# Kernel tuning notes

Hardware: AMD Instinct MI355X
Metric: run time of the kernel (lower is better)

The kernel has to match this reference:

```python
import jax, jax.numpy as jnp
import numpy as np

NUM_QUERIES = 256  # num_queries init arg
D = 256            # decoder_dim


def fps(xyz, n):
    """Furthest point sampling, matching the CUDA furthest_point_sample kernel:
    start at index 0, keep running min squared distance, pick argmax each step.
    xyz: [B, N, 3] -> indices [B, n] int32."""
    B, N, _ = xyz.shape

    def step(carry, _):
        dist, far = carry
        centroid = jnp.take_along_axis(xyz, far[:, None, None], axis=1)  # [B,1,3]
        d = jnp.sum((xyz - centroid) ** 2, axis=-1)                      # [B,N]
        dist = jnp.minimum(dist, d)
        return (dist, jnp.argmax(dist, axis=-1).astype(jnp.int32)), far

    init = (jnp.full((B, N), 1e10, xyz.dtype), jnp.zeros((B,), jnp.int32))
    _, inds = jax.lax.scan(step, init, None, length=n)
    return jnp.transpose(inds)  # [B, n]


def setup_inputs() -> dict:
    key = jax.random.key(0)
    ks = jax.random.split(key, 6)
    B, N = 64, 32768
    # scene coords in roughly [-3, 3]^3 meters
    encoder_xyz = jax.random.uniform(ks[0], (B, N, 3), jnp.float32) * 6.0 - 3.0
    pc_min = jnp.min(encoder_xyz, axis=1)  # [B,3]
    pc_max = jnp.max(encoder_xyz, axis=1)  # [B,3]
    gauss_B = jax.random.normal(ks[1], (3, D // 2), jnp.float32)  # fourier freqs
    W1 = jax.random.normal(ks[2], (D, D), jnp.float32) / np.sqrt(D)
    b1 = jnp.zeros((D,), jnp.float32)
    W2 = jax.random.normal(ks[3], (D, D), jnp.float32) / np.sqrt(D)
    b2 = jnp.zeros((D,), jnp.float32)
    return dict(encoder_xyz=encoder_xyz, pc_min=pc_min, pc_max=pc_max,
                gauss_B=gauss_B, W1=W1, b1=b1, W2=W2, b2=b2)


def reference(encoder_xyz, pc_min, pc_max, gauss_B, W1, b1, W2, b2):
    # --- query selection: FPS + gather (indices are non-differentiable) ---
    inds = fps(jax.lax.stop_gradient(encoder_xyz), NUM_QUERIES)          # [B,nq]
    query_xyz = jnp.take_along_axis(encoder_xyz, inds[..., None], axis=1)  # [B,nq,3]
    # --- PositionEmbeddingCoordsSine (fourier, normalize=True) ---
    norm = (query_xyz - pc_min[:, None, :]) / (pc_max - pc_min)[:, None, :]
    proj = (2.0 * jnp.pi) * jnp.einsum('bnd,df->bnf', norm, gauss_B)     # [B,nq,D/2]
    pos = jnp.concatenate([jnp.sin(proj), jnp.cos(proj)], axis=-1)       # [B,nq,D]
    pos = jnp.transpose(pos, (0, 2, 1))                                   # [B,D,nq]
    # --- query_projection GenericMLP: conv1x1 + ReLU, conv1x1 + output ReLU ---
    h = jax.nn.relu(jnp.einsum('bcn,dc->bdn', pos, W1) + b1[:, None])
    query_embed = jax.nn.relu(jnp.einsum('bcn,dc->bdn', h, W2) + b2[:, None])
    return query_xyz, query_embed
```

## Files before the change

### kernel.cpp

```cpp
#include <hip/hip_runtime.h>

#define FPS_N 32768
#define FPS_T 256
#define NBLK 8
#define PPB (FPS_N / NBLK)
#define PPT (PPB / FPS_T)
#define NCH (PPT / 4)
#define NQ 256
#define DD 256
#define B_BATCH 64
#define FPS_BLOCKS (B_BATCH * NBLK)
#define EMB_BLOCKS (B_BATCH * 4)
#define CHQ 16
#define PLP 20

#define WS_CLEAR_BYTES (B_BATCH * NQ * NBLK * 8)

__global__ __attribute__((amdgpu_flat_work_group_size(FPS_T, FPS_T),
                          amdgpu_waves_per_eu(2, 2)))
void fps_embed_kernel(const float* __restrict__ xyz,
                      const float* __restrict__ pcmin,
                      const float* __restrict__ pcmax,
                      const float* __restrict__ G,
                      const float* __restrict__ W1, const float* __restrict__ b1,
                      const float* __restrict__ W2, const float* __restrict__ b2,
                      float* __restrict__ qout, float* __restrict__ eout,
                      unsigned long long* __restrict__ gslot) {
  const int gid = blockIdx.x;
  const int t = threadIdx.x;

  __shared__ unsigned long long sred[FPS_T / 64];
  __shared__ float4 bc;
  __shared__ __align__(16) float Pl[DD][PLP];
  __shared__ __align__(16) float Hl[DD][PLP];
  __shared__ int swidx[CHQ];
  __shared__ float snrm[CHQ][3];

  if (gid < FPS_BLOCKS) {
    const int xcd = gid & 7;
    const int s = gid >> 3;
    const int b = xcd + 8 * (s >> 3);
    const int q = s & 7;

    const float* __restrict__ base = xyz + (size_t)b * (FPS_N * 3);
    const float4* __restrict__ base4 =
        (const float4*)(base + (size_t)q * PPB * 3) + (size_t)t * (PPT * 3 / 4);
    float* qb = qout + (size_t)b * (NQ * 3);
    unsigned long long* bslot = gslot + (size_t)b * (NQ * NBLK);

    float4 C[PPT * 3 / 4];
#pragma unroll
    for (int i = 0; i < PPT * 3 / 4; ++i) C[i] = base4[i];
#pragma unroll
    for (int i = 0; i < PPT * 3 / 4; ++i) {
      asm volatile("" : "+v"(C[i].x), "+v"(C[i].y), "+v"(C[i].z), "+v"(C[i].w));
    }
    float4 Dst[NCH];
#pragma unroll
    for (int c = 0; c < NCH; ++c) Dst[c] = make_float4(1e10f, 1e10f, 1e10f, 1e10f);

    if (q == 0 && t == 0) { qb[0] = base[0]; qb[1] = base[1]; qb[2] = base[2]; }
    float cx = base[0], cy = base[1], cz = base[2];

#pragma unroll 1
    for (int j = 1; j < NQ; ++j) {
      float best = -1.0f;
      int bik = 0;

#pragma unroll
      for (int c = 0; c < NCH; ++c) {
        const float4 a4 = C[3 * c + 0];
        const float4 b4 = C[3 * c + 1];
        const float4 c4 = C[3 * c + 2];
        const float px[4] = {a4.x, a4.w, b4.z, c4.y};
        const float py[4] = {a4.y, b4.x, b4.w, c4.z};
        const float pz[4] = {a4.z, b4.y, c4.x, c4.w};
        const float dold[4] = {Dst[c].x, Dst[c].y, Dst[c].z, Dst[c].w};
        float dnew[4];
#pragma unroll
        for (int i = 0; i < 4; ++i) {
          const float dx = __fsub_rn(px[i], cx);
          const float dy = __fsub_rn(py[i], cy);
          const float dz = __fsub_rn(pz[i], cz);
          const float d = __fadd_rn(__fadd_rn(__fmul_rn(dx, dx), __fmul_rn(dy, dy)),
                                    __fmul_rn(dz, dz));
          const float nd = fminf(dold[i], d);
          dnew[i] = nd;
          if (nd > best) { best = nd; bik = c * 4 + i; }
        }
        Dst[c] = make_float4(dnew[0], dnew[1], dnew[2], dnew[3]);
      }
      int bi = q * PPB + t * PPT + bik;

#pragma unroll
      for (int off = 32; off; off >>= 1) {
        const float ov = __shfl_xor(best, off);
        const int oi = __shfl_xor(bi, off);
        if (ov > best || (ov == best && oi < bi)) { best = ov; bi = oi; }
      }
      if ((t & 63) == 0) {
        sred[t >> 6] = ((unsigned long long)(unsigned int)__float_as_int(best) << 32) |
                       (unsigned int)~(unsigned int)bi;
      }
      __syncthreads();

      if (t < 64) {
        unsigned long long p = sred[t & 3];
#pragma unroll
        for (int off = 1; off < 4; off <<= 1) {
          const unsigned long long o = __shfl_xor(p, off);
          if (o > p) p = o;
        }
        if (t == 0) {
          __hip_atomic_store(&bslot[j * NBLK + q], p, __ATOMIC_RELAXED,
                             __HIP_MEMORY_SCOPE_AGENT);
        }
        unsigned long long rp = 0;
        if (t < NBLK) {
          const unsigned long long* sl = &bslot[j * NBLK + t];
          do {
            rp = __hip_atomic_load(sl, __ATOMIC_RELAXED, __HIP_MEMORY_SCOPE_AGENT);
          } while (rp == 0ull);
        }
#pragma unroll
        for (int off = 1; off < NBLK; off <<= 1) {
          const unsigned long long o = __shfl_xor(rp, off);
          if (o > rp) rp = o;
        }
        if (t == 0) {
          const int gi = (int)~(unsigned int)(rp & 0xffffffffull);
          const float* cp = base + 3 * (size_t)gi;
          const float ncx = cp[0], ncy = cp[1], ncz = cp[2];
          bc = make_float4(ncx, ncy, ncz, 0.f);
          if (q == 0) { qb[3 * j + 0] = ncx; qb[3 * j + 1] = ncy; qb[3 * j + 2] = ncz; }
        }
      }
      __syncthreads();
      cx = bc.x; cy = bc.y; cz = bc.z;
    }
  } else {
    const int eid = gid - FPS_BLOCKS;
    const int b = eid >> 2;
    const int n0 = (eid & 3) * 64;
    const float* __restrict__ base = xyz + (size_t)b * (FPS_N * 3);
    unsigned long long* bslot = gslot + (size_t)b * (NQ * NBLK);
    float* ob = eout + (size_t)b * (DD * NQ);

    const float mn0 = pcmin[3 * b + 0], mn1 = pcmin[3 * b + 1], mn2 = pcmin[3 * b + 2];
    const float mx0 = pcmax[3 * b + 0], mx1 = pcmax[3 * b + 1], mx2 = pcmax[3 * b + 2];
    const int ty = t >> 2, tx = t & 3;

#pragma unroll 1
    for (int ch = 0; ch < 64 / CHQ; ++ch) {
      const int j0 = n0 + ch * CHQ;
      if (t < NBLK) {
        const unsigned long long* sl = &bslot[(size_t)(j0 + CHQ - 1) * NBLK + t];
        while (__hip_atomic_load(sl, __ATOMIC_RELAXED,
                                 __HIP_MEMORY_SCOPE_AGENT) == 0ull) {
          __builtin_amdgcn_s_sleep(2);
        }
      }
      __syncthreads();
      unsigned long long p = 0xffffffffull;
      if (t < 128) {
        const int line = j0 + (t >> 3);
        if (line > 0) {
          p = __hip_atomic_load(&bslot[(size_t)line * NBLK + (t & 7)],
                                __ATOMIC_RELAXED, __HIP_MEMORY_SCOPE_AGENT);
        }
      }
#pragma unroll
      for (int off = 1; off < 8; off <<= 1) {
        const unsigned long long o = __shfl_xor(p, off);
        if (o > p) p = o;
      }
      if (t < 128 && (t & 7) == 0) {
        swidx[t >> 3] = (int)~(unsigned int)(p & 0xffffffffull);
      }
      __syncthreads();
      if (t < CHQ) {
        const int gi = swidx[t];
        snrm[t][0] = (base[3 * gi + 0] - mn0) / (mx0 - mn0);
        snrm[t][1] = (base[3 * gi + 1] - mn1) / (mx1 - mn1);
        snrm[t][2] = (base[3 * gi + 2] - mn2) / (mx2 - mn2);
      }
      __syncthreads();
      {
        const int qi = t & 15;
        const int fb = t >> 4;
        const float nx = snrm[qi][0], ny = snrm[qi][1], nz = snrm[qi][2];
#pragma unroll
        for (int it = 0; it < 8; ++it) {
          const int f = fb + it * 16;
          const float sfv = nx * G[f] + ny * G[128 + f] + nz * G[256 + f];
          const float pr = 6.28318530717958647692f * sfv;
          Pl[f][qi] = sinf(pr);
          Pl[f + 128][qi] = cosf(pr);
        }
      }
      __syncthreads();
      {
        float acc[4][4] = {};
        const float* wr0 = W1 + (size_t)(ty * 4 + 0) * DD;
        const float* wr1 = wr0 + DD;
        const float* wr2 = wr1 + DD;
        const float* wr3 = wr2 + DD;
#pragma unroll 2
        for (int c = 0; c < DD; c += 4) {
          const float4 a0 = *(const float4*)(wr0 + c);
          const float4 a1 = *(const float4*)(wr1 + c);
          const float4 a2 = *(const float4*)(wr2 + c);
          const float4 a3 = *(const float4*)(wr3 + c);
          const float4 p0 = *(const float4*)&Pl[c + 0][tx * 4];
          const float4 p1 = *(const float4*)&Pl[c + 1][tx * 4];
          const float4 p2 = *(const float4*)&Pl[c + 2][tx * 4];
          const float4 p3 = *(const float4*)&Pl[c + 3][tx * 4];
          const float av[4][4] = {{a0.x, a0.y, a0.z, a0.w},
                                  {a1.x, a1.y, a1.z, a1.w},
                                  {a2.x, a2.y, a2.z, a2.w},
                                  {a3.x, a3.y, a3.z, a3.w}};
          const float pv[4][4] = {{p0.x, p0.y, p0.z, p0.w},
                                  {p1.x, p1.y, p1.z, p1.w},
                                  {p2.x, p2.y, p2.z, p2.w},
                                  {p3.x, p3.y, p3.z, p3.w}};
#pragma unroll
          for (int cj = 0; cj < 4; ++cj)
#pragma unroll
            for (int i = 0; i < 4; ++i)
#pragma unroll
              for (int k = 0; k < 4; ++k)
                acc[i][k] = fmaf(av[i][cj], pv[cj][k], acc[i][k]);
        }
#pragma unroll
        for (int i = 0; i < 4; ++i) {
          const float bv = b1[ty * 4 + i];
          float4 h;
          h.x = fmaxf(acc[i][0] + bv, 0.f);
          h.y = fmaxf(acc[i][1] + bv, 0.f);
          h.z = fmaxf(acc[i][2] + bv, 0.f);
          h.w = fmaxf(acc[i][3] + bv, 0.f);
          *(float4*)&Hl[ty * 4 + i][tx * 4] = h;
        }
      }
      __syncthreads();
      {
        float acc[4][4] = {};
        const float* wr0 = W2 + (size_t)(ty * 4 + 0) * DD;
        const float* wr1 = wr0 + DD;
        const float* wr2 = wr1 + DD;
        const float* wr3 = wr2 + DD;
#pragma unroll 2
        for (int c = 0; c < DD; c += 4) {
          const float4 a0 = *(const float4*)(wr0 + c);
          const float4 a1 = *(const float4*)(wr1 + c);
          const float4 a2 = *(const float4*)(wr2 + c);
          const float4 a3 = *(const float4*)(wr3 + c);
          const float4 p0 = *(const float4*)&Hl[c + 0][tx * 4];
          const float4 p1 = *(const float4*)&Hl[c + 1][tx * 4];
          const float4 p2 = *(const float4*)&Hl[c + 2][tx * 4];
          const float4 p3 = *(const float4*)&Hl[c + 3][tx * 4];
          const float av[4][4] = {{a0.x, a0.y, a0.z, a0.w},
                                  {a1.x, a1.y, a1.z, a1.w},
                                  {a2.x, a2.y, a2.z, a2.w},
                                  {a3.x, a3.y, a3.z, a3.w}};
          const float pv[4][4] = {{p0.x, p0.y, p0.z, p0.w},
                                  {p1.x, p1.y, p1.z, p1.w},
                                  {p2.x, p2.y, p2.z, p2.w},
                                  {p3.x, p3.y, p3.z, p3.w}};
#pragma unroll
          for (int cj = 0; cj < 4; ++cj)
#pragma unroll
            for (int i = 0; i < 4; ++i)
#pragma unroll
              for (int k = 0; k < 4; ++k)
                acc[i][k] = fmaf(av[i][cj], pv[cj][k], acc[i][k]);
        }
#pragma unroll
        for (int i = 0; i < 4; ++i) {
          const float bv = b2[ty * 4 + i];
          float4 h;
          h.x = fmaxf(acc[i][0] + bv, 0.f);
          h.y = fmaxf(acc[i][1] + bv, 0.f);
          h.z = fmaxf(acc[i][2] + bv, 0.f);
          h.w = fmaxf(acc[i][3] + bv, 0.f);
          *(float4*)(ob + (size_t)(ty * 4 + i) * NQ + j0 + tx * 4) = h;
        }
      }
      __syncthreads();
    }
  }
}

extern "C" void kernel_launch(void* const* d_in, const int* in_sizes, int n_in,
                              void* d_out, int out_size, void* d_ws, size_t ws_size,
                              hipStream_t stream) {
  (void)in_sizes; (void)n_in; (void)ws_size; (void)out_size;
  const float* xyz   = (const float*)d_in[0];
  const float* pcmin = (const float*)d_in[1];
  const float* pcmax = (const float*)d_in[2];
  const float* G     = (const float*)d_in[3];
  const float* W1    = (const float*)d_in[4];
  const float* b1    = (const float*)d_in[5];
  const float* W2    = (const float*)d_in[6];
  const float* b2    = (const float*)d_in[7];

  float* qxyz  = (float*)d_out;
  float* embed = qxyz + (size_t)B_BATCH * NQ * 3;

  unsigned long long* gslot = (unsigned long long*)d_ws;

  hipMemsetAsync(d_ws, 0, WS_CLEAR_BYTES, stream);

  hipLaunchKernelGGL(fps_embed_kernel, dim3(FPS_BLOCKS + EMB_BLOCKS),
                     dim3(FPS_T), 0, stream, xyz, pcmin, pcmax, G,
                     W1, b1, W2, b2, qxyz, embed, gslot);
}
```

Baseline: 622.4 us.

## Split fused FPS+embedding kernel into separate FPS and MLP kernels

Replaces the single persistent kernel, where embedding blocks spin-waited on FPS progress slots to overlap the MLP with sampling, with two sequential launches. The FPS kernel now has only its own 512 blocks and no co-resident embedding blocks competing for CUs. The MLP kernel reads the query xyz from the output buffer and processes one 16-query chunk per block across 1024 blocks. This gives up the overlap of MLP work with FPS and adds a second launch, in exchange for removing the polling and contention from the FPS critical path.

```diff
diff --git a/kernel.cpp b/kernel.cpp
--- a/kernel.cpp
+++ b/kernel.cpp
@@ -9,8 +9,6 @@
 #define NQ 256
 #define DD 256
 #define B_BATCH 64
-#define FPS_BLOCKS (B_BATCH * NBLK)
-#define EMB_BLOCKS (B_BATCH * 4)
 #define CHQ 16
 #define PLP 20
 
@@ -18,275 +16,244 @@
 
 __global__ __attribute__((amdgpu_flat_work_group_size(FPS_T, FPS_T),
                           amdgpu_waves_per_eu(2, 2)))
-void fps_embed_kernel(const float* __restrict__ xyz,
-                      const float* __restrict__ pcmin,
-                      const float* __restrict__ pcmax,
-                      const float* __restrict__ G,
-                      const float* __restrict__ W1, const float* __restrict__ b1,
-                      const float* __restrict__ W2, const float* __restrict__ b2,
-                      float* __restrict__ qout, float* __restrict__ eout,
-                      unsigned long long* __restrict__ gslot) {
+void fps_kernel(const float* __restrict__ xyz, float* __restrict__ qout,
+                unsigned long long* __restrict__ gslot) {
   const int gid = blockIdx.x;
+  const int xcd = gid & 7;
+  const int s = gid >> 3;
+  const int b = xcd + 8 * (s >> 3);
+  const int q = s & 7;
   const int t = threadIdx.x;
+
+  const float* __restrict__ base = xyz + (size_t)b * (FPS_N * 3);
+  const float4* __restrict__ base4 =
+      (const float4*)(base + (size_t)q * PPB * 3) + (size_t)t * (PPT * 3 / 4);
+  float* qb = qout + (size_t)b * (NQ * 3);
+  unsigned long long* bslot = gslot + (size_t)b * (NQ * NBLK);
 
   __shared__ unsigned long long sred[FPS_T / 64];
   __shared__ float4 bc;
+
+  float4 C[PPT * 3 / 4];
+#pragma unroll
+  for (int i = 0; i < PPT * 3 / 4; ++i) C[i] = base4[i];
+#pragma unroll
+  for (int i = 0; i < PPT * 3 / 4; ++i) {
+    asm volatile("" : "+v"(C[i].x), "+v"(C[i].y), "+v"(C[i].z), "+v"(C[i].w));
+  }
+  float4 Dst[NCH];
+#pragma unroll
+  for (int c = 0; c < NCH; ++c) Dst[c] = make_float4(1e10f, 1e10f, 1e10f, 1e10f);
+
+  if (q == 0 && t == 0) { qb[0] = base[0]; qb[1] = base[1]; qb[2] = base[2]; }
+  float cx = base[0], cy = base[1], cz = base[2];
+
+#pragma unroll 1
+  for (int j = 1; j < NQ; ++j) {
+    float best = -1.0f;
+    int bik = 0;
+
+#pragma unroll
+    for (int c = 0; c < NCH; ++c) {
+      const float4 a4 = C[3 * c + 0];
+      const float4 b4 = C[3 * c + 1];
+      const float4 c4 = C[3 * c + 2];
+      const float px[4] = {a4.x, a4.w, b4.z, c4.y};
+      const float py[4] = {a4.y, b4.x, b4.w, c4.z};
+      const float pz[4] = {a4.z, b4.y, c4.x, c4.w};
+      const float dold[4] = {Dst[c].x, Dst[c].y, Dst[c].z, Dst[c].w};
+      float dnew[4];
+#pragma unroll
+      for (int i = 0; i < 4; ++i) {
+        const float dx = __fsub_rn(px[i], cx);
+        const float dy = __fsub_rn(py[i], cy);
+        const float dz = __fsub_rn(pz[i], cz);
+        const float d = __fadd_rn(__fadd_rn(__fmul_rn(dx, dx), __fmul_rn(dy, dy)),
+                                  __fmul_rn(dz, dz));
+        const float nd = fminf(dold[i], d);
+        dnew[i] = nd;
+        if (nd > best) { best = nd; bik = c * 4 + i; }
+      }
+      Dst[c] = make_float4(dnew[0], dnew[1], dnew[2], dnew[3]);
+    }
+    int bi = q * PPB + t * PPT + bik;
+
+#pragma unroll
+    for (int off = 32; off; off >>= 1) {
+      const float ov = __shfl_xor(best, off);
+      const int oi = __shfl_xor(bi, off);
+      if (ov > best || (ov == best && oi < bi)) { best = ov; bi = oi; }
+    }
+    if ((t & 63) == 0) {
+      sred[t >> 6] = ((unsigned long long)(unsigned int)__float_as_int(best) << 32) |
+                     (unsigned int)~(unsigned int)bi;
+    }
+    __syncthreads();
+
+    if (t < 64) {
+      unsigned long long p = sred[t & 3];
+#pragma unroll
+      for (int off = 1; off < 4; off <<= 1) {
+        const unsigned long long o = __shfl_xor(p, off);
+        if (o > p) p = o;
+      }
+      if (t == 0) {
+        __hip_atomic_store(&bslot[j * NBLK + q], p, __ATOMIC_RELAXED,
+                           __HIP_MEMORY_SCOPE_AGENT);
+      }
+      unsigned long long rp = 0;
+      if (t < NBLK) {
+        const unsigned long long* sl = &bslot[j * NBLK + t];
+        do {
+          rp = __hip_atomic_load(sl, __ATOMIC_RELAXED, __HIP_MEMORY_SCOPE_AGENT);
+        } while (rp == 0ull);
+      }
+#pragma unroll
+      for (int off = 1; off < NBLK; off <<= 1) {
+        const unsigned long long o = __shfl_xor(rp, off);
+        if (o > rp) rp = o;
+      }
+      if (t == 0) {
+        const int gi = (int)~(unsigned int)(rp & 0xffffffffull);
+        const float* cp = base + 3 * (size_t)gi;
+        const float ncx = cp[0], ncy = cp[1], ncz = cp[2];
+        bc = make_float4(ncx, ncy, ncz, 0.f);
+        if (q == 0) { qb[3 * j + 0] = ncx; qb[3 * j + 1] = ncy; qb[3 * j + 2] = ncz; }
+      }
+    }
+    __syncthreads();
+    cx = bc.x; cy = bc.y; cz = bc.z;
+  }
+}
+
+__global__ __launch_bounds__(256) void embed_mlp_kernel(
+    const float* __restrict__ qxyz, const float* __restrict__ pcmin,
+    const float* __restrict__ pcmax, const float* __restrict__ G,
+    const float* __restrict__ W1, const float* __restrict__ b1,
+    const float* __restrict__ W2, const float* __restrict__ b2,
+    float* __restrict__ out) {
+  const int eid = blockIdx.x;
+  const int b = eid >> 4;
+  const int j0 = (eid & 15) * CHQ;
+  const int t = threadIdx.x;
+  const int ty = t >> 2, tx = t & 3;
+
   __shared__ __align__(16) float Pl[DD][PLP];
   __shared__ __align__(16) float Hl[DD][PLP];
-  __shared__ int swidx[CHQ];
   __shared__ float snrm[CHQ][3];
 
-  if (gid < FPS_BLOCKS) {
-    const int xcd = gid & 7;
-    const int s = gid >> 3;
-    const int b = xcd + 8 * (s >> 3);
-    const int q = s & 7;
-
-    const float* __restrict__ base = xyz + (size_t)b * (FPS_N * 3);
-    const float4* __restrict__ base4 =
-        (const float4*)(base + (size_t)q * PPB * 3) + (size_t)t * (PPT * 3 / 4);
-    float* qb = qout + (size_t)b * (NQ * 3);
-    unsigned long long* bslot = gslot + (size_t)b * (NQ * NBLK);
-
-    float4 C[PPT * 3 / 4];
-#pragma unroll
-    for (int i = 0; i < PPT * 3 / 4; ++i) C[i] = base4[i];
-#pragma unroll
-    for (int i = 0; i < PPT * 3 / 4; ++i) {
-      asm volatile("" : "+v"(C[i].x), "+v"(C[i].y), "+v"(C[i].z), "+v"(C[i].w));
-    }
-    float4 Dst[NCH];
-#pragma unroll
-    for (int c = 0; c < NCH; ++c) Dst[c] = make_float4(1e10f, 1e10f, 1e10f, 1e10f);
-
-    if (q == 0 && t == 0) { qb[0] = base[0]; qb[1] = base[1]; qb[2] = base[2]; }
-    float cx = base[0], cy = base[1], cz = base[2];
-
-#pragma unroll 1
-    for (int j = 1; j < NQ; ++j) {
-      float best = -1.0f;
-      int bik = 0;
-
-#pragma unroll
-      for (int c = 0; c < NCH; ++c) {
-        const float4 a4 = C[3 * c + 0];
-        const float4 b4 = C[3 * c + 1];
-        const float4 c4 = C[3 * c + 2];
-        const float px[4] = {a4.x, a4.w, b4.z, c4.y};
-        const float py[4] = {a4.y, b4.x, b4.w, c4.z};
-        const float pz[4] = {a4.z, b4.y, c4.x, c4.w};
-        const float dold[4] = {Dst[c].x, Dst[c].y, Dst[c].z, Dst[c].w};
-        float dnew[4];
-#pragma unroll
-        for (int i = 0; i < 4; ++i) {
-          const float dx = __fsub_rn(px[i], cx);
-          const float dy = __fsub_rn(py[i], cy);
-          const float dz = __fsub_rn(pz[i], cz);
-          const float d = __fadd_rn(__fadd_rn(__fmul_rn(dx, dx), __fmul_rn(dy, dy)),
-                                    __fmul_rn(dz, dz));
-          const float nd = fminf(dold[i], d);
-          dnew[i] = nd;
-          if (nd > best) { best = nd; bik = c * 4 + i; }
-        }
-        Dst[c] = make_float4(dnew[0], dnew[1], dnew[2], dnew[3]);
-      }
-      int bi = q * PPB + t * PPT + bik;
-
-#pragma unroll
-      for (int off = 32; off; off >>= 1) {
-        const float ov = __shfl_xor(best, off);
-        const int oi = __shfl_xor(bi, off);
-        if (ov > best || (ov == best && oi < bi)) { best = ov; bi = oi; }
-      }
-      if ((t & 63) == 0) {
-        sred[t >> 6] = ((unsigned long long)(unsigned int)__float_as_int(best) << 32) |
-                       (unsigned int)~(unsigned int)bi;
-      }
-      __syncthreads();
-
-      if (t < 64) {
-        unsigned long long p = sred[t & 3];
-#pragma unroll
-        for (int off = 1; off < 4; off <<= 1) {
-          const unsigned long long o = __shfl_xor(p, off);
-          if (o > p) p = o;
-        }
-        if (t == 0) {
-          __hip_atomic_store(&bslot[j * NBLK + q], p, __ATOMIC_RELAXED,
-                             __HIP_MEMORY_SCOPE_AGENT);
-        }
-        unsigned long long rp = 0;
-        if (t < NBLK) {
-          const unsigned long long* sl = &bslot[j * NBLK + t];
-          do {
-            rp = __hip_atomic_load(sl, __ATOMIC_RELAXED, __HIP_MEMORY_SCOPE_AGENT);
-          } while (rp == 0ull);
-        }
-#pragma unroll
-        for (int off = 1; off < NBLK; off <<= 1) {
-          const unsigned long long o = __shfl_xor(rp, off);
-          if (o > rp) rp = o;
-        }
-        if (t == 0) {
-          const int gi = (int)~(unsigned int)(rp & 0xffffffffull);
-          const float* cp = base + 3 * (size_t)gi;
-          const float ncx = cp[0], ncy = cp[1], ncz = cp[2];
-          bc = make_float4(ncx, ncy, ncz, 0.f);
-          if (q == 0) { qb[3 * j + 0] = ncx; qb[3 * j + 1] = ncy; qb[3 * j + 2] = ncz; }
-        }
-      }
-      __syncthreads();
-      cx = bc.x; cy = bc.y; cz = bc.z;
-    }
-  } else {
-    const int eid = gid - FPS_BLOCKS;
-    const int b = eid >> 2;
-    const int n0 = (eid & 3) * 64;
-    const float* __restrict__ base = xyz + (size_t)b * (FPS_N * 3);
-    unsigned long long* bslot = gslot + (size_t)b * (NQ * NBLK);
-    float* ob = eout + (size_t)b * (DD * NQ);
-
-    const float mn0 = pcmin[3 * b + 0], mn1 = pcmin[3 * b + 1], mn2 = pcmin[3 * b + 2];
-    const float mx0 = pcmax[3 * b + 0], mx1 = pcmax[3 * b + 1], mx2 = pcmax[3 * b + 2];
-    const int ty = t >> 2, tx = t & 3;
-
-#pragma unroll 1
-    for (int ch = 0; ch < 64 / CHQ; ++ch) {
-      const int j0 = n0 + ch * CHQ;
-      if (t < NBLK) {
-        const unsigned long long* sl = &bslot[(size_t)(j0 + CHQ - 1) * NBLK + t];
-        while (__hip_atomic_load(sl, __ATOMIC_RELAXED,
-                                 __HIP_MEMORY_SCOPE_AGENT) == 0ull) {
-          __builtin_amdgcn_s_sleep(2);
-        }
-      }
-      __syncthreads();
-      unsigned long long p = 0xffffffffull;
-      if (t < 128) {
-        const int line = j0 + (t >> 3);
-        if (line > 0) {
-          p = __hip_atomic_load(&bslot[(size_t)line * NBLK + (t & 7)],
-                                __ATOMIC_RELAXED, __HIP_MEMORY_SCOPE_AGENT);
-        }
-      }
-#pragma unroll
-      for (int off = 1; off < 8; off <<= 1) {
-        const unsigned long long o = __shfl_xor(p, off);
-        if (o > p) p = o;
-      }
-      if (t < 128 && (t & 7) == 0) {
-        swidx[t >> 3] = (int)~(unsigned int)(p & 0xffffffffull);
-      }
-      __syncthreads();
-      if (t < CHQ) {
-        const int gi = swidx[t];
-        snrm[t][0] = (base[3 * gi + 0] - mn0) / (mx0 - mn0);
-        snrm[t][1] = (base[3 * gi + 1] - mn1) / (mx1 - mn1);
-        snrm[t][2] = (base[3 * gi + 2] - mn2) / (mx2 - mn2);
-      }
-      __syncthreads();
-      {
-        const int qi = t & 15;
-        const int fb = t >> 4;
-        const float nx = snrm[qi][0], ny = snrm[qi][1], nz = snrm[qi][2];
-#pragma unroll
-        for (int it = 0; it < 8; ++it) {
-          const int f = fb + it * 16;
-          const float sfv = nx * G[f] + ny * G[128 + f] + nz * G[256 + f];
-          const float pr = 6.28318530717958647692f * sfv;
-          Pl[f][qi] = sinf(pr);
-          Pl[f + 128][qi] = cosf(pr);
-        }
-      }
-      __syncthreads();
-      {
-        float acc[4][4] = {};
-        const float* wr0 = W1 + (size_t)(ty * 4 + 0) * DD;
-        const float* wr1 = wr0 + DD;
-        const float* wr2 = wr1 + DD;
-        const float* wr3 = wr2 + DD;
+  const float* qb = qxyz + (size_t)b * (NQ * 3);
+  float* ob = out + (size_t)b * (DD * NQ);
+
+  if (t < CHQ) {
+    const int n = j0 + t;
+    snrm[t][0] = (qb[3 * n + 0] - pcmin[3 * b + 0]) / (pcmax[3 * b + 0] - pcmin[3 * b + 0]);
+    snrm[t][1] = (qb[3 * n + 1] - pcmin[3 * b + 1]) / (pcmax[3 * b + 1] - pcmin[3 * b + 1]);
+    snrm[t][2] = (qb[3 * n + 2] - pcmin[3 * b + 2]) / (pcmax[3 * b + 2] - pcmin[3 * b + 2]);
+  }
+  __syncthreads();
+
+  {
+    const int qi = t & 15;
+    const int fb = t >> 4;
+    const float nx = snrm[qi][0], ny = snrm[qi][1], nz = snrm[qi][2];
+#pragma unroll
+    for (int it = 0; it < 8; ++it) {
+      const int f = fb + it * 16;
+      const float sfv = nx * G[f] + ny * G[128 + f] + nz * G[256 + f];
+      const float pr = 6.28318530717958647692f * sfv;
+      Pl[f][qi] = sinf(pr);
+      Pl[f + 128][qi] = cosf(pr);
+    }
+  }
+  __syncthreads();
+
+  {
+    float acc[4][4] = {};
+    const float* wr0 = W1 + (size_t)(ty * 4 + 0) * DD;
+    const float* wr1 = wr0 + DD;
+    const float* wr2 = wr1 + DD;
+    const float* wr3 = wr2 + DD;
 #pragma unroll 2
-        for (int c = 0; c < DD; c += 4) {
-          const float4 a0 = *(const float4*)(wr0 + c);
-          const float4 a1 = *(const float4*)(wr1 + c);
-          const float4 a2 = *(const float4*)(wr2 + c);
-          const float4 a3 = *(const float4*)(wr3 + c);
-          const float4 p0 = *(const float4*)&Pl[c + 0][tx * 4];
-          const float4 p1 = *(const float4*)&Pl[c + 1][tx * 4];
-          const float4 p2 = *(const float4*)&Pl[c + 2][tx * 4];
-          const float4 p3 = *(const float4*)&Pl[c + 3][tx * 4];
-          const float av[4][4] = {{a0.x, a0.y, a0.z, a0.w},
-                                  {a1.x, a1.y, a1.z, a1.w},
-                                  {a2.x, a2.y, a2.z, a2.w},
-                                  {a3.x, a3.y, a3.z, a3.w}};
-          const float pv[4][4] = {{p0.x, p0.y, p0.z, p0.w},
-                                  {p1.x, p1.y, p1.z, p1.w},
-                                  {p2.x, p2.y, p2.z, p2.w},
-                                  {p3.x, p3.y, p3.z, p3.w}};
-#pragma unroll
-          for (int cj = 0; cj < 4; ++cj)
-#pragma unroll
-            for (int i = 0; i < 4; ++i)
-#pragma unroll
-              for (int k = 0; k < 4; ++k)
-                acc[i][k] = fmaf(av[i][cj], pv[cj][k], acc[i][k]);
-        }
-#pragma unroll
-        for (int i = 0; i < 4; ++i) {
-          const float bv = b1[ty * 4 + i];
-          float4 h;
-          h.x = fmaxf(acc[i][0] + bv, 0.f);
-          h.y = fmaxf(acc[i][1] + bv, 0.f);
-          h.z = fmaxf(acc[i][2] + bv, 0.f);
-          h.w = fmaxf(acc[i][3] + bv, 0.f);
-          *(float4*)&Hl[ty * 4 + i][tx * 4] = h;
-        }
-      }
-      __syncthreads();
-      {
-        float acc[4][4] = {};
-        const float* wr0 = W2 + (size_t)(ty * 4 + 0) * DD;
-        const float* wr1 = wr0 + DD;
-        const float* wr2 = wr1 + DD;
-        const float* wr3 = wr2 + DD;
+    for (int c = 0; c < DD; c += 4) {
+      const float4 a0 = *(const float4*)(wr0 + c);
+      const float4 a1 = *(const float4*)(wr1 + c);
+      const float4 a2 = *(const float4*)(wr2 + c);
+      const float4 a3 = *(const float4*)(wr3 + c);
+      const float4 p0 = *(const float4*)&Pl[c + 0][tx * 4];
+      const float4 p1 = *(const float4*)&Pl[c + 1][tx * 4];
+      const float4 p2 = *(const float4*)&Pl[c + 2][tx * 4];
+      const float4 p3 = *(const float4*)&Pl[c + 3][tx * 4];
+      const float av[4][4] = {{a0.x, a0.y, a0.z, a0.w},
+                              {a1.x, a1.y, a1.z, a1.w},
+                              {a2.x, a2.y, a2.z, a2.w},
+                              {a3.x, a3.y, a3.z, a3.w}};
+      const float pv[4][4] = {{p0.x, p0.y, p0.z, p0.w},
+                              {p1.x, p1.y, p1.z, p1.w},
+                              {p2.x, p2.y, p2.z, p2.w},
+                              {p3.x, p3.y, p3.z, p3.w}};
+#pragma unroll
+      for (int cj = 0; cj < 4; ++cj)
+#pragma unroll
+        for (int i = 0; i < 4; ++i)
+#pragma unroll
+          for (int k = 0; k < 4; ++k)
+            acc[i][k] = fmaf(av[i][cj], pv[cj][k], acc[i][k]);
+    }
+#pragma unroll
+    for (int i = 0; i < 4; ++i) {
+      const float bv = b1[ty * 4 + i];
+      float4 h;
+      h.x = fmaxf(acc[i][0] + bv, 0.f);
+      h.y = fmaxf(acc[i][1] + bv, 0.f);
+      h.z = fmaxf(acc[i][2] + bv, 0.f);
+      h.w = fmaxf(acc[i][3] + bv, 0.f);
+      *(float4*)&Hl[ty * 4 + i][tx * 4] = h;
+    }
+  }
+  __syncthreads();
+
+  {
+    float acc[4][4] = {};
+    const float* wr0 = W2 + (size_t)(ty * 4 + 0) * DD;
+    const float* wr1 = wr0 + DD;
+    const float* wr2 = wr1 + DD;
+    const float* wr3 = wr2 + DD;
 #pragma unroll 2
-        for (int c = 0; c < DD; c += 4) {
-          const float4 a0 = *(const float4*)(wr0 + c);
-          const float4 a1 = *(const float4*)(wr1 + c);
-          const float4 a2 = *(const float4*)(wr2 + c);
-          const float4 a3 = *(const float4*)(wr3 + c);
-          const float4 p0 = *(const float4*)&Hl[c + 0][tx * 4];
-          const float4 p1 = *(const float4*)&Hl[c + 1][tx * 4];
-          const float4 p2 = *(const float4*)&Hl[c + 2][tx * 4];
-          const float4 p3 = *(const float4*)&Hl[c + 3][tx * 4];
-          const float av[4][4] = {{a0.x, a0.y, a0.z, a0.w},
-                                  {a1.x, a1.y, a1.z, a1.w},
-                                  {a2.x, a2.y, a2.z, a2.w},
-                                  {a3.x, a3.y, a3.z, a3.w}};
-          const float pv[4][4] = {{p0.x, p0.y, p0.z, p0.w},
-                                  {p1.x, p1.y, p1.z, p1.w},
-                                  {p2.x, p2.y, p2.z, p2.w},
-                                  {p3.x, p3.y, p3.z, p3.w}};
-#pragma unroll
-          for (int cj = 0; cj < 4; ++cj)
-#pragma unroll
-            for (int i = 0; i < 4; ++i)
-#pragma unroll
-              for (int k = 0; k < 4; ++k)
-                acc[i][k] = fmaf(av[i][cj], pv[cj][k], acc[i][k]);
-        }
-#pragma unroll
-        for (int i = 0; i < 4; ++i) {
-          const float bv = b2[ty * 4 + i];
-          float4 h;
-          h.x = fmaxf(acc[i][0] + bv, 0.f);
-          h.y = fmaxf(acc[i][1] + bv, 0.f);
-          h.z = fmaxf(acc[i][2] + bv, 0.f);
-          h.w = fmaxf(acc[i][3] + bv, 0.f);
-          *(float4*)(ob + (size_t)(ty * 4 + i) * NQ + j0 + tx * 4) = h;
-        }
-      }
-      __syncthreads();
+    for (int c = 0; c < DD; c += 4) {
+      const float4 a0 = *(const float4*)(wr0 + c);
+      const float4 a1 = *(const float4*)(wr1 + c);
+      const float4 a2 = *(const float4*)(wr2 + c);
+      const float4 a3 = *(const float4*)(wr3 + c);
+      const float4 p0 = *(const float4*)&Hl[c + 0][tx * 4];
+      const float4 p1 = *(const float4*)&Hl[c + 1][tx * 4];
+      const float4 p2 = *(const float4*)&Hl[c + 2][tx * 4];
+      const float4 p3 = *(const float4*)&Hl[c + 3][tx * 4];
+      const float av[4][4] = {{a0.x, a0.y, a0.z, a0.w},
+                              {a1.x, a1.y, a1.z, a1.w},
+                              {a2.x, a2.y, a2.z, a2.w},
+                              {a3.x, a3.y, a3.z, a3.w}};
+      const float pv[4][4] = {{p0.x, p0.y, p0.z, p0.w},
+                              {p1.x, p1.y, p1.z, p1.w},
+                              {p2.x, p2.y, p2.z, p2.w},
+                              {p3.x, p3.y, p3.z, p3.w}};
+#pragma unroll
+      for (int cj = 0; cj < 4; ++cj)
+#pragma unroll
+        for (int i = 0; i < 4; ++i)
+#pragma unroll
+          for (int k = 0; k < 4; ++k)
+            acc[i][k] = fmaf(av[i][cj], pv[cj][k], acc[i][k]);
+    }
+#pragma unroll
+    for (int i = 0; i < 4; ++i) {
+      const float bv = b2[ty * 4 + i];
+      float4 h;
+      h.x = fmaxf(acc[i][0] + bv, 0.f);
+      h.y = fmaxf(acc[i][1] + bv, 0.f);
+      h.z = fmaxf(acc[i][2] + bv, 0.f);
+      h.w = fmaxf(acc[i][3] + bv, 0.f);
+      *(float4*)(ob + (size_t)(ty * 4 + i) * NQ + j0 + tx * 4) = h;
     }
   }
 }
@@ -311,7 +278,8 @@
 
   hipMemsetAsync(d_ws, 0, WS_CLEAR_BYTES, stream);
 
-  hipLaunchKernelGGL(fps_embed_kernel, dim3(FPS_BLOCKS + EMB_BLOCKS),
-                     dim3(FPS_T), 0, stream, xyz, pcmin, pcmax, G,
-                     W1, b1, W2, b2, qxyz, embed, gslot);
+  hipLaunchKernelGGL(fps_kernel, dim3(B_BATCH * NBLK), dim3(FPS_T), 0, stream,
+                     xyz, qxyz, gslot);
+  hipLaunchKernelGGL(embed_mlp_kernel, dim3(B_BATCH * 16), dim3(256), 0, stream,
+                     qxyz, pcmin, pcmax, G, W1, b1, W2, b2, embed);
 }
```

After: 576.6 us. 7.4% less time.
